# Kernel tuning notes

Measured on AMD Instinct MI355X. Metric: run time of the kernel, lower is better.

Reference implementation:

```python
import jax, jax.numpy as jnp
import numpy as np

B, N, C, F = 64, 64, 8, 256      # batch, neighbors per sample, in_channels, in_features
OC, OF = 8, 256                  # out_channels, out_features


def setup_inputs() -> dict:
    key = jax.random.key(0)
    k0, k1, k2, k3, k4 = jax.random.split(key, 5)
    x = jax.random.normal(k0, (B, C, F), dtype=jnp.float32)
    neighbor = jax.random.normal(k1, (B, N, C, F), dtype=jnp.float32)
    # att1/att2: nn.Linear(in_features, in_channels, bias=False) -> weight (C, F)
    W1 = jax.random.normal(k2, (C, F), dtype=jnp.float32) * (1.0 / np.sqrt(F))
    W2 = jax.random.normal(k3, (C, F), dtype=jnp.float32) * (1.0 / np.sqrt(F))
    # conv: nn.Conv1d(C, OC*OF, kernel_size=F, bias=False) -> weight (OC*OF, C, F)
    Wc = jax.random.normal(k4, (OC * OF, C, F), dtype=jnp.float32) * (1.0 / np.sqrt(C * F))
    return {"x": x, "neighbor": neighbor, "W1": W1, "W2": W2, "Wc": Wc}


def _sgnroot(a):
    return jnp.sign(a) * jnp.sqrt(jnp.clip(jnp.abs(a), 1e-8))


def _row_normalize(a):
    # torch: x / (x.abs().sum(1, keepdim=True) + 1e-7); dim 1 is the channel dim of (B,C,F,F)
    a = a / (jnp.abs(a).sum(axis=1, keepdims=True) + 1e-7)
    return jnp.where(jnp.isnan(a), 0.0, a)


def _feature_adjacency(x, neighbor, W1, W2):
    # w[b,n] = sum_{c,k} (x[b] @ W1^T)[c,k] * sum_{k,l} (neighbor[b,n] @ W2^T)[k,l]
    s1 = jnp.einsum('bcf,kf->b', x, W1)            # total sum of att1(x[b])
    s2 = jnp.einsum('bncf,kf->bn', neighbor, W2)   # total sum of att2(y[b,n])
    w = s1[:, None] * s2                            # (B, N)
    # fadj[b,c,a,d] = sum_n x[b,c,a] * neighbor[b,n,c,d] * w[b,n]
    fadj = jnp.einsum('bca,bncd,bn->bcad', x, neighbor, w)
    fadj = fadj + jnp.swapaxes(fadj, -2, -1)
    return _row_normalize(_sgnroot(fadj))


def _conv_transform(z, Wc, lead_shape):
    # Conv1d(C, OC*OF, kernel_size=F, bias=False) over (.., C, F) == full contraction
    out = jnp.einsum('...cf,ocf->...o', z, Wc)
    return out.reshape(*lead_shape, OC, OF)


def reference(x, neighbor, W1, W2, Wc):
    adj = _feature_adjacency(x, neighbor, W1, W2)              # (B,C,F,F)
    # transform(x, adj): (adj @ x.unsqueeze(-1)).squeeze(-1) then conv
    zx = jnp.einsum('bcad,bcd->bca', adj, x)                   # (B,C,F)
    x_out = _conv_transform(zx, Wc, (x.shape[0],))             # (B,OC,OF)
    # transform(neighbor[i], adj[i:i+1]) for each i -> adj broadcasts over N
    zn = jnp.einsum('bcad,bncd->bnca', adj, neighbor)          # (B,N,C,F)
    n_out = _conv_transform(zn, Wc, (x.shape[0], neighbor.shape[1]))  # (B,N,OC,OF)
    return x_out, n_out
```

## Files before the change

kernel.cpp:

```cpp
#include <hip/hip_runtime.h>
#include <hip/hip_bf16.h>
#include <math.h>

#define B_ 64
#define N_ 64
#define C_ 8
#define F_ 256
#define K_ 2048
#define NO_ 2048
#define M_TOT 4160

typedef __attribute__((ext_vector_type(8))) short bf16x8;
typedef __attribute__((ext_vector_type(4))) float f32x4;

__device__ __forceinline__ unsigned short bfbits(float f) {
    union { __hip_bfloat16 h; unsigned short u; } cv;
    cv.h = __float2bfloat16(f);
    return cv.u;
}

__global__ __launch_bounds__(256) void sums_wc_k(const float* __restrict__ x,
        const float* __restrict__ nb, const float* __restrict__ W1,
        const float* __restrict__ W2, const float* __restrict__ Wc,
        float* __restrict__ s1, float* __restrict__ s2,
        __hip_bfloat16* __restrict__ Bbuf) {
    int blk = blockIdx.x;
    int f = threadIdx.x;
    if (blk >= B_ * N_ + B_) {
        int i = (blk - (B_ * N_ + B_)) * 1024 + f * 4;
        float4 v = *(const float4*)(Wc + i);
        ushort4 u = { bfbits(v.x), bfbits(v.y), bfbits(v.z), bfbits(v.w) };
        *(ushort4*)(&Bbuf[i]) = u;
        return;
    }
    float val;
    if (blk < B_ * N_) {
        const float* base = nb + (size_t)blk * (C_ * F_);
        float wsum = 0.f;
        #pragma unroll
        for (int k = 0; k < C_; ++k) wsum += W2[k * F_ + f];
        float cs = 0.f;
        #pragma unroll
        for (int c = 0; c < C_; ++c) cs += base[c * F_ + f];
        val = cs * wsum;
    } else {
        int b = blk - B_ * N_;
        const float* base = x + (size_t)b * (C_ * F_);
        float wsum = 0.f;
        #pragma unroll
        for (int k = 0; k < C_; ++k) wsum += W1[k * F_ + f];
        float cs = 0.f;
        #pragma unroll
        for (int c = 0; c < C_; ++c) cs += base[c * F_ + f];
        val = cs * wsum;
    }
    #pragma unroll
    for (int off = 32; off > 0; off >>= 1) val += __shfl_down(val, off, 64);
    __shared__ float wred[4];
    int w = f >> 6;
    if ((f & 63) == 0) wred[w] = val;
    __syncthreads();
    if (f == 0) {
        float s = wred[0] + wred[1] + wred[2] + wred[3];
        if (blk < B_ * N_) s2[blk] = s;
        else s1[blk - B_ * N_] = s;
    }
}

__global__ __launch_bounds__(1024) void t_k(const float* __restrict__ nb,
        const float* __restrict__ s1, const float* __restrict__ s2,
        float* __restrict__ t) {
    int blk = blockIdx.x;
    int b = blk / C_, c = blk % C_;
    int tid = threadIdx.x;
    int q = tid >> 8, d = tid & 255;
    const float* p = nb + ((size_t)(b * N_) * C_ + c) * F_ + d;
    const float* s2p = s2 + b * N_;
    float acc = 0.f;
    #pragma unroll
    for (int j = 0; j < 16; ++j) {
        int n = q * 16 + j;
        acc += p[(size_t)n * C_ * F_] * s2p[n];
    }
    __shared__ float part[4][F_];
    part[q][d] = acc;
    __syncthreads();
    if (tid < 256) {
        float s = part[0][d] + part[1][d] + part[2][d] + part[3][d];
        t[(size_t)blk * F_ + d] = s * s1[b];
    }
}

__global__ __launch_bounds__(256) void denom_k(const float* __restrict__ x,
        const float* __restrict__ t, float* __restrict__ rdenom) {
    int blk = blockIdx.x;
    int b = blk >> 8, a = blk & 255;
    int d = threadIdx.x;
    float acc = 1e-7f;
    #pragma unroll
    for (int c = 0; c < C_; ++c) {
        size_t o = ((size_t)b * C_ + c) * F_;
        float xa = x[o + a], ta = t[o + a];
        float xd = x[o + d], td = t[o + d];
        float v = xa * td + xd * ta;
        float r = __builtin_amdgcn_sqrtf(fmaxf(fabsf(v), 1e-8f));
        acc += (v != 0.f) ? r : 0.f;
    }
    rdenom[(size_t)blk * F_ + d] = __builtin_amdgcn_rcpf(acc);
}

__device__ __forceinline__ float sgnroot_dev(float v) {
    float r = __builtin_amdgcn_sqrtf(fmaxf(fabsf(v), 1e-8f));
    return (v > 0.f) ? r : ((v < 0.f) ? -r : 0.f);
}

#define ZNX_PAD 264
__global__ __launch_bounds__(256, 2) void znx_k(const float* __restrict__ x,
        const float* __restrict__ t, const float* __restrict__ rdenom,
        const float* __restrict__ nb, __hip_bfloat16* __restrict__ Abuf) {
    int bc = blockIdx.x;
    int b = bc >> 3, c = bc & 7;
    int tid = threadIdx.x;
    int wave = tid >> 6, lane = tid & 63;
    __shared__ float xs[F_], ts[F_];
    __shared__ __hip_bfloat16 nbB[80 * ZNX_PAD];

    xs[tid] = x[(size_t)bc * F_ + tid];
    ts[tid] = t[(size_t)bc * F_ + tid];
    {
        int r = tid >> 2, cs0 = (tid & 3) * 64;
        const float* src = nb + (((size_t)(b * N_ + r)) * C_ + c) * F_ + cs0;
        __hip_bfloat16* dst = nbB + r * ZNX_PAD + cs0;
        #pragma unroll
        for (int j = 0; j < 64; j += 4) {
            float4 v = *(const float4*)(src + j);
            ushort4 u = { bfbits(v.x), bfbits(v.y), bfbits(v.z), bfbits(v.w) };
            *(ushort4*)(&dst[j]) = u;
        }
    }
    if (tid < 64) {
        float4 v = *(const float4*)(x + (size_t)bc * F_ + tid * 4);
        ushort4 u = { bfbits(v.x), bfbits(v.y), bfbits(v.z), bfbits(v.w) };
        *(ushort4*)(&nbB[64 * ZNX_PAD + tid * 4]) = u;
    }
    {
        __hip_bfloat16 z = __float2bfloat16(0.f);
        #pragma unroll
        for (int j = 0; j < 16; ++j) {
            int o = 65 * ZNX_PAD + tid * 16 + j;
            if (o < 80 * ZNX_PAD) nbB[o] = z;
        }
    }
    __syncthreads();

    const int aq = lane & 15;
    const int dq = lane >> 4;
    f32x4 acc[4][5] = {};
    #pragma unroll
    for (int atile = 0; atile < 4; ++atile) {
        int a = wave * 64 + atile * 16 + aq;
        float xa = xs[a], ta = ts[a];
        const float* drow = rdenom + ((size_t)b * F_ + a) * F_;
        #pragma unroll
        for (int kc = 0; kc < 8; ++kc) {
            int d0 = kc * 32 + dq * 8;
            float4 xv0 = *(const float4*)(xs + d0);
            float4 xv1 = *(const float4*)(xs + d0 + 4);
            float4 tv0 = *(const float4*)(ts + d0);
            float4 tv1 = *(const float4*)(ts + d0 + 4);
            float4 dn0 = *(const float4*)(drow + d0);
            float4 dn1 = *(const float4*)(drow + d0 + 4);
            float xv[8] = {xv0.x, xv0.y, xv0.z, xv0.w, xv1.x, xv1.y, xv1.z, xv1.w};
            float tv[8] = {tv0.x, tv0.y, tv0.z, tv0.w, tv1.x, tv1.y, tv1.z, tv1.w};
            float dn[8] = {dn0.x, dn0.y, dn0.z, dn0.w, dn1.x, dn1.y, dn1.z, dn1.w};
            union { bf16x8 v; __hip_bfloat16 h[8]; } bu;
            #pragma unroll
            for (int j = 0; j < 8; ++j) {
                float g = sgnroot_dev(xa * tv[j] + xv[j] * ta);
                bu.h[j] = __float2bfloat16(g * dn[j]);
            }
            #pragma unroll
            for (int mt = 0; mt < 5; ++mt) {
                bf16x8 af = *(const bf16x8*)(nbB + (mt * 16 + aq) * ZNX_PAD
                                             + kc * 32 + dq * 8);
                acc[atile][mt] = __builtin_amdgcn_mfma_f32_16x16x32_bf16(
                    af, bu.v, acc[atile][mt], 0, 0, 0);
            }
        }
    }

    __syncthreads();
    #pragma unroll
    for (int atile = 0; atile < 4; ++atile) {
        int a = wave * 64 + atile * 16 + aq;
        #pragma unroll
        for (int mt = 0; mt < 4; ++mt) {
            #pragma unroll
            for (int i = 0; i < 4; ++i) {
                int n = mt * 16 + dq * 4 + i;
                nbB[n * ZNX_PAD + a] = __float2bfloat16(acc[atile][mt][i]);
            }
        }
        if (dq == 0)
            nbB[64 * ZNX_PAD + a] = __float2bfloat16(acc[atile][4][0]);
    }
    __syncthreads();
    for (int it = 0; it < 17; ++it) {
        int q = it * 256 + tid;
        if (q < 4160) {
            int row = q >> 6;
            int off = (q & 63) * 4;
            ushort4 u = *(const ushort4*)(&nbB[row * ZNX_PAD + off]);
            int grow = (row < 64) ? (64 + b * N_ + row) : b;
            *(ushort4*)(&Abuf[(size_t)grow * K_ + c * F_ + off]) = u;
        }
    }
}

__global__ __launch_bounds__(256) void gemm_bf16_k(
        const __hip_bfloat16* __restrict__ A,
        const __hip_bfloat16* __restrict__ Bm,
        float* __restrict__ Cm) {
    __shared__ char lds[49152] __attribute__((aligned(16)));
    const int t = threadIdx.x;
    const int wave = t >> 6;
    const int lane = t & 63;
    const int col0 = blockIdx.x * 128;
    const int row0 = blockIdx.y * 128;
    const int wrow0 = (wave & 1) * 64;
    const int wcol0 = (wave >> 1) * 64;
    const int aq = lane & 15;
    const int dq = lane >> 4;

    const int rA0 = t >> 2;
    const int kcs = ((t & 3) - ((t >> 3) & 3)) & 3;
    const int kc = kcs * 8;
    const int grA0 = min(row0 + rA0, M_TOT - 1);
    const int grA1 = min(row0 + rA0 + 64, M_TOT - 1);
    const int gcB0 = col0 + rA0;
    const int gcB1 = col0 + rA0 + 64;
    const size_t aoff0 = (size_t)grA0 * K_ + kc;
    const size_t aoff1 = (size_t)grA1 * K_ + kc;
    const size_t boff0 = (size_t)gcB0 * K_ + kc;
    const size_t boff1 = (size_t)gcB1 * K_ + kc;
    const int swz = ((dq + (aq >> 1)) & 3) * 16;
    const int ldsw = wave * 1024;

    f32x4 acc[4][4] = {};

#define STAGE(BI, TK) do {                                                     \
    const int k0_ = (TK) * 32;                                                 \
    char* la_ = lds + (BI) * 16384 + ldsw;                                     \
    char* lb_ = la_ + 8192;                                                    \
    __builtin_amdgcn_global_load_lds(                                          \
        (const __attribute__((address_space(1))) void*)(A + aoff0 + k0_),      \
        (__attribute__((address_space(3))) void*)la_, 16, 0, 0);               \
    __builtin_amdgcn_global_load_lds(                                          \
        (const __attribute__((address_space(1))) void*)(A + aoff1 + k0_),      \
        (__attribute__((address_space(3))) void*)(la_ + 4096), 16, 0, 0);      \
    __builtin_amdgcn_global_load_lds(                                          \
        (const __attribute__((address_space(1))) void*)(Bm + boff0 + k0_),     \
        (__attribute__((address_space(3))) void*)lb_, 16, 0, 0);               \
    __builtin_amdgcn_global_load_lds(                                          \
        (const __attribute__((address_space(1))) void*)(Bm + boff1 + k0_),     \
        (__attribute__((address_space(3))) void*)(lb_ + 4096), 16, 0, 0);      \
} while (0)

#define COMPUTE(BI) do {                                                       \
    const char* la_ = lds + (BI) * 16384;                                      \
    const char* lb_ = la_ + 8192;                                              \
    bf16x8 af_[4], bf_[4];                                                     \
    _Pragma("unroll")                                                          \
    for (int rb = 0; rb < 4; ++rb)                                             \
        af_[rb] = *(const bf16x8*)(la_ + (wrow0 + rb * 16 + aq) * 64 + swz);   \
    _Pragma("unroll")                                                          \
    for (int cb = 0; cb < 4; ++cb)                                             \
        bf_[cb] = *(const bf16x8*)(lb_ + (wcol0 + cb * 16 + aq) * 64 + swz);   \
    __builtin_amdgcn_s_setprio(1);                                             \
    _Pragma("unroll")                                                          \
    for (int rb = 0; rb < 4; ++rb)                                             \
        _Pragma("unroll")                                                      \
        for (int cb = 0; cb < 4; ++cb)                                         \
            acc[rb][cb] = __builtin_amdgcn_mfma_f32_16x16x32_bf16(             \
                af_[rb], bf_[cb], acc[rb][cb], 0, 0, 0);                       \
    __builtin_amdgcn_s_setprio(0);                                             \
} while (0)

#define WAIT_PIPE(N) do {                                                      \
    asm volatile("s_waitcnt vmcnt(" #N ")" ::: "memory");                      \
    __builtin_amdgcn_sched_barrier(0);                                         \
    __builtin_amdgcn_s_barrier();                                              \
    __builtin_amdgcn_sched_barrier(0);                                         \
} while (0)

    STAGE(0, 0);
    STAGE(1, 1);
    STAGE(2, 2);

    for (int t3 = 0; t3 < 60; t3 += 3) {
        WAIT_PIPE(8);
        COMPUTE(0);
        __builtin_amdgcn_s_barrier();
        STAGE(0, t3 + 3);

        WAIT_PIPE(8);
        COMPUTE(1);
        __builtin_amdgcn_s_barrier();
        STAGE(1, t3 + 4);

        WAIT_PIPE(8);
        COMPUTE(2);
        __builtin_amdgcn_s_barrier();
        STAGE(2, t3 + 5);
    }
    WAIT_PIPE(8);
    COMPUTE(0);
    __builtin_amdgcn_s_barrier();
    STAGE(0, 63);
    WAIT_PIPE(8);
    COMPUTE(1);
    WAIT_PIPE(4);
    COMPUTE(2);
    WAIT_PIPE(0);
    COMPUTE(0);

#undef STAGE
#undef COMPUTE
#undef WAIT_PIPE

    #pragma unroll
    for (int rb = 0; rb < 4; ++rb) {
        int rowbase = row0 + wrow0 + rb * 16 + (lane >> 4) * 4;
        #pragma unroll
        for (int cb = 0; cb < 4; ++cb) {
            int col = col0 + wcol0 + cb * 16 + (lane & 15);
            #pragma unroll
            for (int i = 0; i < 4; ++i) {
                int row = rowbase + i;
                if (row < M_TOT)
                    Cm[(size_t)row * NO_ + col] = acc[rb][cb][i];
            }
        }
    }
}

extern "C" void kernel_launch(void* const* d_in, const int* in_sizes, int n_in,
                              void* d_out, int out_size, void* d_ws, size_t ws_size,
                              hipStream_t stream) {
    const float* x  = (const float*)d_in[0];
    const float* nb = (const float*)d_in[1];
    const float* W1 = (const float*)d_in[2];
    const float* W2 = (const float*)d_in[3];
    const float* Wc = (const float*)d_in[4];
    float* out = (float*)d_out;
    float* ws = (float*)d_ws;

    float* s1    = ws;
    float* s2    = ws + 64;
    float* t     = ws + 4160;
    float* rden  = ws + 135232;
    __hip_bfloat16* Abuf = (__hip_bfloat16*)(ws + 4329536);
    __hip_bfloat16* Bbuf = Abuf + (size_t)M_TOT * K_;

    hipLaunchKernelGGL(sums_wc_k, dim3(B_ * N_ + B_ + (K_ * NO_) / 1024),
                       dim3(256), 0, stream, x, nb, W1, W2, Wc, s1, s2, Bbuf);
    hipLaunchKernelGGL(t_k, dim3(B_ * C_), dim3(1024), 0, stream, nb, s1, s2, t);
    hipLaunchKernelGGL(denom_k, dim3(B_ * F_), dim3(256), 0, stream, x, t, rden);
    hipLaunchKernelGGL(znx_k, dim3(B_ * C_), dim3(256), 0, stream,
                       x, t, rden, nb, Abuf);
    hipLaunchKernelGGL(gemm_bf16_k, dim3(16, 33), dim3(256), 0, stream,
                       Abuf, Bbuf, out);
}
```

Before: 209.3 us.

## Software-pipeline LDS fragment reads with double-buffered registers in bf16 GEMM

```diff
diff --git a/kernel.cpp b/kernel.cpp
--- a/kernel.cpp
+++ b/kernel.cpp
@@ -217,7 +217,7 @@
     }
 }
 
-__global__ __launch_bounds__(256) void gemm_bf16_k(
+__global__ __launch_bounds__(256, 3) void gemm_bf16_k(
         const __hip_bfloat16* __restrict__ A,
         const __hip_bfloat16* __restrict__ Bm,
         float* __restrict__ Cm) {
@@ -247,6 +247,7 @@
     const int ldsw = wave * 1024;
 
     f32x4 acc[4][4] = {};
+    bf16x8 afr[2][4], bfr[2][4];
 
 #define STAGE(BI, TK) do {                                                     \
     const int k0_ = (TK) * 32;                                                 \
@@ -266,67 +267,80 @@
         (__attribute__((address_space(3))) void*)(lb_ + 4096), 16, 0, 0);      \
 } while (0)
 
-#define COMPUTE(BI) do {                                                       \
+#define DSREAD(BI, RI) do {                                                    \
     const char* la_ = lds + (BI) * 16384;                                      \
     const char* lb_ = la_ + 8192;                                              \
-    bf16x8 af_[4], bf_[4];                                                     \
     _Pragma("unroll")                                                          \
     for (int rb = 0; rb < 4; ++rb)                                             \
-        af_[rb] = *(const bf16x8*)(la_ + (wrow0 + rb * 16 + aq) * 64 + swz);   \
+        afr[RI][rb] = *(const bf16x8*)(la_ + (wrow0 + rb * 16 + aq) * 64 + swz);\
     _Pragma("unroll")                                                          \
     for (int cb = 0; cb < 4; ++cb)                                             \
-        bf_[cb] = *(const bf16x8*)(lb_ + (wcol0 + cb * 16 + aq) * 64 + swz);   \
-    __builtin_amdgcn_s_setprio(1);                                             \
+        bfr[RI][cb] = *(const bf16x8*)(lb_ + (wcol0 + cb * 16 + aq) * 64 + swz);\
+} while (0)
+
+#define MFMAS(RI) do {                                                         \
     _Pragma("unroll")                                                          \
     for (int rb = 0; rb < 4; ++rb)                                             \
         _Pragma("unroll")                                                      \
         for (int cb = 0; cb < 4; ++cb)                                         \
             acc[rb][cb] = __builtin_amdgcn_mfma_f32_16x16x32_bf16(             \
-                af_[rb], bf_[cb], acc[rb][cb], 0, 0, 0);                       \
-    __builtin_amdgcn_s_setprio(0);                                             \
-} while (0)
-
-#define WAIT_PIPE(N) do {                                                      \
+                afr[RI][rb], bfr[RI][cb], acc[rb][cb], 0, 0, 0);               \
+} while (0)
+
+#define WAITV(N) do {                                                          \
     asm volatile("s_waitcnt vmcnt(" #N ")" ::: "memory");                      \
     __builtin_amdgcn_sched_barrier(0);                                         \
     __builtin_amdgcn_s_barrier();                                              \
     __builtin_amdgcn_sched_barrier(0);                                         \
 } while (0)
 
+#define LGKM8BAR do {                                                          \
+    asm volatile("s_waitcnt lgkmcnt(8)" ::: "memory");                         \
+    __builtin_amdgcn_sched_barrier(0);                                         \
+    __builtin_amdgcn_s_barrier();                                              \
+    __builtin_amdgcn_sched_barrier(0);                                         \
+} while (0)
+
+#define SLOT(BN, RN, BS, RC, TKS) do {                                         \
+    WAITV(4);                                                                  \
+    DSREAD(BN, RN);                                                            \
+    LGKM8BAR;                                                                  \
+    STAGE(BS, TKS);                                                            \
+    MFMAS(RC);                                                                 \
+} while (0)
+
     STAGE(0, 0);
     STAGE(1, 1);
     STAGE(2, 2);
-
-    for (int t3 = 0; t3 < 60; t3 += 3) {
-        WAIT_PIPE(8);
-        COMPUTE(0);
-        __builtin_amdgcn_s_barrier();
-        STAGE(0, t3 + 3);
-
-        WAIT_PIPE(8);
-        COMPUTE(1);
-        __builtin_amdgcn_s_barrier();
-        STAGE(1, t3 + 4);
-
-        WAIT_PIPE(8);
-        COMPUTE(2);
-        __builtin_amdgcn_s_barrier();
-        STAGE(2, t3 + 5);
-    }
-    WAIT_PIPE(8);
-    COMPUTE(0);
+    asm volatile("s_waitcnt vmcnt(8)" ::: "memory");
+    __builtin_amdgcn_sched_barrier(0);
     __builtin_amdgcn_s_barrier();
-    STAGE(0, 63);
-    WAIT_PIPE(8);
-    COMPUTE(1);
-    WAIT_PIPE(4);
-    COMPUTE(2);
-    WAIT_PIPE(0);
-    COMPUTE(0);
+    __builtin_amdgcn_sched_barrier(0);
+    DSREAD(0, 0);
+
+    for (int s6 = 0; s6 < 60; s6 += 6) {
+        SLOT(1, 1, 0, 0, s6 + 3);
+        SLOT(2, 0, 1, 1, s6 + 4);
+        SLOT(0, 1, 2, 0, s6 + 5);
+        SLOT(1, 0, 0, 1, s6 + 6);
+        SLOT(2, 1, 1, 0, s6 + 7);
+        SLOT(0, 0, 2, 1, s6 + 8);
+    }
+    SLOT(1, 1, 0, 0, 63);
+    WAITV(4);
+    DSREAD(2, 0);
+    MFMAS(1);
+    WAITV(0);
+    DSREAD(0, 1);
+    MFMAS(0);
+    MFMAS(1);
 
 #undef STAGE
-#undef COMPUTE
-#undef WAIT_PIPE
+#undef DSREAD
+#undef MFMAS
+#undef WAITV
+#undef LGKM8BAR
+#undef SLOT
 
     #pragma unroll
     for (int rb = 0; rb < 4; ++rb) {
```

New measurement: 205.7 us. No clear change (-1.7%).
